# Kernel optimization log

Hardware: AMD Instinct MI355X
Metric: run time of the kernel (lower is better)

## Reference

```python
import jax, jax.numpy as jnp
import numpy as np

NUM_HEADS = 3
WIN = 7            # window_size (square)
PAD = WIN // 2     # conv / v padding


def setup_inputs() -> dict:
    key = jax.random.key(0)
    ks = jax.random.split(key, 8)
    B, C, H, W = 8, 96, 56, 56
    hd = C // NUM_HEADS  # 32
    x = jax.random.normal(ks[0], (B, C, H, W), jnp.float32)
    # qkv 1x1 conv: weight (3C, C), bias (3C,)
    w_qkv = jax.random.normal(ks[1], (3 * C, C), jnp.float32) * (C ** -0.5)
    b_qkv = jax.random.normal(ks[2], (3 * C,), jnp.float32) * 0.01
    fan_in = 2 * hd * WIN * WIN
    w_dm = jax.random.normal(ks[3], (WIN * WIN, 2 * hd, WIN, WIN), jnp.float32) * (fan_in ** -0.5)
    b_dm = jax.random.normal(ks[4], (WIN * WIN,), jnp.float32) * 0.01
    bias_table = jax.random.normal(ks[5], (WIN * WIN, NUM_HEADS), jnp.float32) * 0.02
    # proj 1x1 conv
    w_proj = jax.random.normal(ks[6], (C, C), jnp.float32) * (C ** -0.5)
    b_proj = jax.random.normal(ks[7], (C,), jnp.float32) * 0.01
    return dict(x=x, w_qkv=w_qkv, b_qkv=b_qkv, w_dm=w_dm, b_dm=b_dm,
                bias_table=bias_table, w_proj=w_proj, b_proj=b_proj)


def reference(x, w_qkv, b_qkv, w_dm, b_dm, bias_table, w_proj, b_proj):
    B, C, H, W = x.shape
    nh = NUM_HEADS
    hd = C // nh
    scale = hd ** -0.5

    # qkv 1x1 conv -> (B, 3, nh, hd, H, W)
    qkv = jnp.einsum('oc,bchw->bohw', w_qkv, x) + b_qkv[None, :, None, None]
    qkv = qkv.reshape(B, 3, nh, hd, H, W)
    q, k, v = qkv[:, 0], qkv[:, 1], qkv[:, 2]

    qk = jnp.concatenate([(q * scale).reshape(B * nh, hd, H, W),
                          k.reshape(B * nh, hd, H, W)], axis=1)
    attn = jax.lax.conv_general_dilated(
        qk, w_dm, window_strides=(1, 1), padding=[(PAD, PAD), (PAD, PAD)],
        dimension_numbers=('NCHW', 'OIHW', 'NCHW')) + b_dm[None, :, None, None]
    attn = attn.reshape(B, nh, WIN * WIN, H, W)

    # relative position bias, broadcast over spatial dims
    attn = attn + bias_table.T.reshape(1, nh, WIN * WIN, 1, 1)
    attn = jax.nn.softmax(attn, axis=2)

    # gather sliding windows of v from a zero-padded tensor
    v_pad = jnp.pad(v, ((0, 0), (0, 0), (0, 0), (PAD, PAD), (PAD, PAD)))
    vw = jnp.stack([v_pad[..., i // WIN:i // WIN + H, i % WIN:i % WIN + W]
                    for i in range(WIN * WIN)], axis=3)

    # weighted sum over window dim, merge heads back to channels
    out = jnp.sum(vw * attn[:, :, None], axis=3).reshape(B, C, H, W)

    # output 1x1 projection (dropout p=0 -> identity)
    out = jnp.einsum('oc,bchw->bohw', w_proj, out) + b_proj[None, :, None, None]
    return out
```

## Files before the change

kernel.cpp:

```cpp
#include <hip/hip_runtime.h>
#include <hip/hip_bf16.h>
#include <stdint.h>

#define BATCH 8
#define CCH 96
#define NH 3
#define HD 32
#define HGT 56
#define WID 56
#define HW 3136
#define WIN 7
#define KK 49
#define PADR 3
#define NIMG 24
#define C2 64

typedef const float* fp32p;
typedef __attribute__((ext_vector_type(8))) short bf16x8;
typedef __attribute__((ext_vector_type(16))) float f32x16;
typedef unsigned short ushort_t;

__device__ __forceinline__ float bf2f_bits(unsigned u){ return __uint_as_float(u << 16); }
__device__ __forceinline__ ushort_t f2bf_bits(float f){
  __hip_bfloat16 hb = __float2bfloat16(f);
  return *(ushort_t*)&hb;
}

__global__ void prep_kernel(fp32p w_dm, fp32p b_dm, fp32p bias_table,
                            fp32p w_qkv, fp32p w_proj,
                            __hip_bfloat16* __restrict__ w3, float* __restrict__ bias3,
                            ushort_t* __restrict__ wq3, ushort_t* __restrict__ wp3){
  int t = blockIdx.x * 256 + threadIdx.x;
  if (t < 200704){
    int j   = t & 7;
    int l   = (t >> 3) & 63;
    int mt  = (t >> 9) & 1;
    int cb  = (t >> 10) & 1;
    int pt  = t >> 11;
    int pass = pt / KK, tap = pt % KK;
    int o  = mt*32 + (l & 31);
    int ch = pass*32 + cb*16 + (l >> 5)*8 + j;
    float v = 0.f;
    if (o < KK) v = w_dm[((size_t)(o*C2 + ch))*KK + tap];
    w3[t] = __float2bfloat16(v);
  } else if (t < 200896){
    int t2 = t - 200704;
    int h = t2 >> 6;
    int o = t2 & 63;
    bias3[t2] = (o < KK) ? (b_dm[o] + bias_table[o*NH + h]) : -1e30f;
  } else if (t < 200896 + 27648){
    int i = t - 200896;
    int j = i & 7, l = (i >> 3) & 63;
    int rest = i >> 9;
    int mt = rest % 9, k = rest / 9;
    int o = mt*32 + (l & 31);
    int c = k*16 + (l >> 5)*8 + j;
    wq3[i] = f2bf_bits(w_qkv[o*CCH + c]);
  } else if (t < 200896 + 27648 + 9216){
    int i = t - 200896 - 27648;
    int j = i & 7, l = (i >> 3) & 63;
    int rest = i >> 9;
    int mt = rest % 3, k = rest / 3;
    int o = mt*32 + (l & 31);
    int c = k*16 + (l >> 5)*8 + j;
    wp3[i] = f2bf_bits(w_proj[o*CCH + c]);
  }
}

__global__ __launch_bounds__(256) void xt_kernel(fp32p x, ushort_t* __restrict__ xbf){
  __shared__ float lds[128*97];
  int px0 = blockIdx.x * 128;
  int tid = threadIdx.x;
  #pragma unroll
  for (int it = 0; it < 48; ++it){
    int s = tid + it*256;
    int px = s & 127;
    int c  = s >> 7;
    int gpx = px0 + px;
    int b = gpx / HW, pp = gpx % HW;
    lds[px*97 + c] = x[((size_t)b*CCH + c)*HW + pp];
  }
  __syncthreads();
  #pragma unroll
  for (int it = 0; it < 6; ++it){
    int s = tid + it*256;
    int j  = s % 12;
    int px = s / 12;
    unsigned u[4];
    #pragma unroll
    for (int q = 0; q < 4; ++q){
      float f0 = lds[px*97 + j*8 + 2*q];
      float f1 = lds[px*97 + j*8 + 2*q + 1];
      u[q] = (unsigned)f2bf_bits(f0) | ((unsigned)f2bf_bits(f1) << 16);
    }
    uint4 w4; w4.x=u[0]; w4.y=u[1]; w4.z=u[2]; w4.w=u[3];
    *(uint4*)((char*)xbf + ((size_t)(px0+px)*96 + j*8)*2) = w4;
  }
}

__global__ __launch_bounds__(64) void qkv_kernel(const ushort_t* __restrict__ xbf,
    const ushort_t* __restrict__ wq3, fp32p b_qkv,
    ushort_t* __restrict__ qplane, ushort_t* __restrict__ kplane,
    ushort_t* __restrict__ v2){
  int wid = blockIdx.x;
  int g  = wid / 784;
  int pt = wid % 784;
  int l = threadIdx.x & 63, col = l & 31, hi = l >> 5;
  int px = pt*32 + col;
  int b = px / HW, pp = px % HW;

  bf16x8 B[6];
  const char* bb = (const char*)xbf + (size_t)px*192 + hi*16;
  #pragma unroll
  for (int k = 0; k < 6; ++k) B[k] = *(const bf16x8*)(bb + k*32);

  f32x16 acc[3];
  #pragma unroll
  for (int m = 0; m < 3; ++m)
    #pragma unroll
    for (int r = 0; r < 16; ++r) acc[m][r] = 0.f;

  #pragma unroll
  for (int k = 0; k < 6; ++k){
    #pragma unroll
    for (int m = 0; m < 3; ++m){
      bf16x8 A = *(const bf16x8*)((const char*)wq3 + ((size_t)((k*9 + g*3 + m)*64 + l))*16);
      acc[m] = __builtin_amdgcn_mfma_f32_32x32x16_bf16(A, B[k], acc[m], 0, 0, 0);
    }
  }
  const float scale = 0.17677669529663687f;
  ushort_t* plane = (g == 0) ? qplane : (g == 1 ? kplane : v2);
  #pragma unroll
  for (int m = 0; m < 3; ++m){
    ushort_t* dst = plane + ((size_t)((b*NH + m)*HW + pp))*32;
    #pragma unroll
    for (int q = 0; q < 4; ++q){
      int base = 8*q + 4*hi;
      float v0 = acc[m][q*4+0] + b_qkv[g*96 + m*32 + base + 0];
      float v1 = acc[m][q*4+1] + b_qkv[g*96 + m*32 + base + 1];
      float v2f = acc[m][q*4+2] + b_qkv[g*96 + m*32 + base + 2];
      float v3 = acc[m][q*4+3] + b_qkv[g*96 + m*32 + base + 3];
      if (g == 0){ v0 *= scale; v1 *= scale; v2f *= scale; v3 *= scale; }
      uint2 pk;
      pk.x = (unsigned)f2bf_bits(v0) | ((unsigned)f2bf_bits(v1) << 16);
      pk.y = (unsigned)f2bf_bits(v2f) | ((unsigned)f2bf_bits(v3) << 16);
      *(uint2*)(&dst[base]) = pk;
    }
  }
}

#define MFMA4(Ab, Bb) \
  { _Pragma("unroll") for (int cb = 0; cb < 2; ++cb){ \
      acc[0] = __builtin_amdgcn_mfma_f32_32x32x16_bf16(Ab[cb][0], Bb[cb], acc[0], 0, 0, 0); \
      acc[1] = __builtin_amdgcn_mfma_f32_32x32x16_bf16(Ab[cb][1], Bb[cb], acc[1], 0, 0, 0); \
    } }

#define LOADA(tt, Ab) \
  { const char* An_ = Abase + (size_t)(tt)*4096; \
    _Pragma("unroll") for (int cb = 0; cb < 2; ++cb) \
      _Pragma("unroll") for (int mt = 0; mt < 2; ++mt) \
        Ab[cb][mt] = *(const bf16x8*)(An_ + (cb*2 + mt)*1024); }

#define LOADB(tt, Bb) \
  { int ky_ = (tt) / 7, kx_ = (tt) - ky_*7; \
    int xp_ = nth*32 + col + kx_; if (xp_ > 61) xp_ = 61; \
    int base_ = ((row + ky_)*64 + xp_)*64; \
    int sx_ = (xp_ & 3) ^ ((xp_ >> 2) & 3); \
    _Pragma("unroll") for (int cb = 0; cb < 2; ++cb) \
      Bb[cb] = *(const bf16x8*)(&smem[base_ + ((((cb << 1) | hi) ^ sx_) << 4)]); }

__global__ __launch_bounds__(256, 3) void attn_kernel(
    const ushort_t* __restrict__ qplane, const ushort_t* __restrict__ kplane,
    const __hip_bfloat16* __restrict__ w3, const float* __restrict__ bias3,
    const ushort_t* __restrict__ v2, ushort_t* __restrict__ tmp2){
  __shared__ char smem[49664];

  int bid = blockIdx.x;
  int n  = bid / 28;
  int y0 = (bid % 28) * 2;
  int b = n / NH, head = n % NH;
  int tid = threadIdx.x;
  int l = tid & 63, w = tid >> 6, hi = l >> 5, col = l & 31;
  int row = w >> 1;
  int nth = w & 1;

  f32x16 acc[2];
  #pragma unroll
  for (int r = 0; r < 16; ++r){
    int rowv = (r & 3) + 8*(r >> 2) + 4*hi;
    acc[0][r] = bias3[head*64 + rowv];
    acc[1][r] = bias3[head*64 + 32 + rowv];
  }

  for (int pass = 0; pass < 2; ++pass){
    if (pass) __syncthreads();
    const char* src = (const char*)(pass ? kplane : qplane) + (size_t)n * HW * 64;
    #pragma unroll
    for (int it = 0; it < 8; ++it){
      int s = tid + it*256;
      int c   = s & 3;
      int xp  = (s >> 2) & 63;
      int rw  = s >> 8;
      int gy = y0 - 3 + rw;
      int gx = xp - 3;
      uint4 val = {0,0,0,0};
      if ((unsigned)gy < HGT && (unsigned)gx < WID)
        val = *(const uint4*)(src + (size_t)(gy*WID + gx)*64 + c*16);
      int sw = (c ^ (xp & 3) ^ ((xp >> 2) & 3)) << 4;
      *(uint4*)(&smem[(rw*64 + xp)*64 + sw]) = val;
    }
    __syncthreads();

    const char* Abase = (const char*)w3 + (size_t)pass*KK*4096 + l*16;
    bf16x8 A0[2][2], A1[2][2], B0[2], B1[2];
    LOADA(0, A0); LOADB(0, B0);
    LOADA(1, A1); LOADB(1, B1);
    for (int t = 0; t < 48; t += 2){
      MFMA4(A0, B0);
      LOADA(t+2, A0); LOADB(t+2, B0);
      MFMA4(A1, B1);
      int t3 = (t+3 < KK) ? (t+3) : 48;
      LOADA(t3, A1); LOADB(t3, B1);
    }
    MFMA4(A0, B0);
  }

  ushort_t* Pp = (ushort_t*)&smem[32768];
  {
    float m = -1e30f;
    #pragma unroll
    for (int r = 0; r < 16; ++r){ m = fmaxf(m, acc[0][r]); m = fmaxf(m, acc[1][r]); }
    m = fmaxf(m, __shfl_xor(m, 32));
    float s = 0.f;
    #pragma unroll
    for (int r = 0; r < 16; ++r){
      acc[0][r] = __expf(acc[0][r] - m); s += acc[0][r];
      acc[1][r] = __expf(acc[1][r] - m); s += acc[1][r];
    }
    s += __shfl_xor(s, 32);
    float inv = 1.f / s;
    int pixslot = row*64 + nth*32 + col;
    #pragma unroll
    for (int r = 0; r < 16; ++r){
      int rowv = (r & 3) + 8*(r >> 2) + 4*hi;
      Pp[pixslot*66 + rowv] = f2bf_bits(acc[0][r] * inv);
      int o1 = 32 + rowv;
      if (o1 < KK) Pp[pixslot*66 + o1] = f2bf_bits(acc[1][r] * inv);
    }
  }
  __syncthreads();

  const char* vb = (const char*)v2 + (size_t)n * HW * 64;
  #pragma unroll
  for (int it = 0; it < 8; ++it){
    int s = tid + it*256;
    int xp  = s & 63;
    int c   = (s >> 6) & 3;
    int rw  = s >> 8;
    int gy = y0 - 3 + rw;
    int gx = xp - 3;
    uint4 val = {0,0,0,0};
    if ((unsigned)gy < HGT && (unsigned)gx < WID)
      val = *(const uint4*)(vb + (size_t)(gy*WID + gx)*64 + c*16);
    *(uint4*)(&smem[((c*8 + rw)*64 + xp)*16]) = val;
  }
  __syncthreads();

  int ch2 = tid >> 7;
  int slot = tid & 127;
  int pr = slot >> 6, pxx = slot & 63;
  if (pxx < WID){
    float out[16];
    #pragma unroll
    for (int i = 0; i < 16; ++i) out[i] = 0.f;
    #pragma unroll
    for (int ky = 0; ky < WIN; ++ky){
      #pragma unroll
      for (int kx = 0; kx < WIN; ++kx){
        float pw = bf2f_bits(Pp[slot*66 + ky*7 + kx]);
        int vrow = pr + ky, xp = pxx + kx;
        #pragma unroll
        for (int ci = 0; ci < 2; ++ci){
          int cc = ch2*2 + ci;
          uint4 vv = *(const uint4*)(&smem[((cc*8 + vrow)*64 + xp)*16]);
          unsigned ua[4] = {vv.x, vv.y, vv.z, vv.w};
          #pragma unroll
          for (int q = 0; q < 4; ++q){
            out[ci*8 + 2*q]     = fmaf(pw, __uint_as_float(ua[q] << 16),         out[ci*8 + 2*q]);
            out[ci*8 + 2*q + 1] = fmaf(pw, __uint_as_float(ua[q] & 0xffff0000u), out[ci*8 + 2*q + 1]);
          }
        }
      }
    }
    int pp = (y0 + pr)*WID + pxx;
    ushort_t* dst = tmp2 + ((size_t)(b*HW + pp))*96 + head*32 + ch2*16;
    #pragma unroll
    for (int j2 = 0; j2 < 2; ++j2){
      unsigned u[4];
      #pragma unroll
      for (int q = 0; q < 4; ++q){
        u[q] = (unsigned)f2bf_bits(out[j2*8 + 2*q]) | ((unsigned)f2bf_bits(out[j2*8 + 2*q + 1]) << 16);
      }
      uint4 w4; w4.x=u[0]; w4.y=u[1]; w4.z=u[2]; w4.w=u[3];
      *(uint4*)(&dst[j2*8]) = w4;
    }
  }
}

__global__ __launch_bounds__(64) void proj_kernel(const ushort_t* __restrict__ tmp2,
    const ushort_t* __restrict__ wp3, fp32p b_proj, float* __restrict__ outp){
  int pt = blockIdx.x;
  int l = threadIdx.x & 63, col = l & 31, hi = l >> 5;
  int px = pt*32 + col;
  int b = px / HW, pp = px % HW;

  bf16x8 B[6];
  const char* bb = (const char*)tmp2 + (size_t)px*192 + hi*16;
  #pragma unroll
  for (int k = 0; k < 6; ++k) B[k] = *(const bf16x8*)(bb + k*32);

  f32x16 acc[3];
  #pragma unroll
  for (int m = 0; m < 3; ++m)
    #pragma unroll
    for (int r = 0; r < 16; ++r) acc[m][r] = 0.f;

  #pragma unroll
  for (int k = 0; k < 6; ++k){
    #pragma unroll
    for (int m = 0; m < 3; ++m){
      bf16x8 A = *(const bf16x8*)((const char*)wp3 + ((size_t)((k*3 + m)*64 + l))*16);
      acc[m] = __builtin_amdgcn_mfma_f32_32x32x16_bf16(A, B[k], acc[m], 0, 0, 0);
    }
  }
  #pragma unroll
  for (int m = 0; m < 3; ++m){
    #pragma unroll
    for (int r = 0; r < 16; ++r){
      int o = m*32 + (r & 3) + 8*(r >> 2) + 4*hi;
      outp[((size_t)(b*CCH + o))*HW + pp] = acc[m][r] + b_proj[o];
    }
  }
}

extern "C" void kernel_launch(void* const* d_in, const int* in_sizes, int n_in,
                              void* d_out, int out_size, void* d_ws, size_t ws_size,
                              hipStream_t stream){
  fp32p x          = (fp32p)d_in[0];
  fp32p w_qkv      = (fp32p)d_in[1];
  fp32p b_qkv      = (fp32p)d_in[2];
  fp32p w_dm       = (fp32p)d_in[3];
  fp32p b_dm       = (fp32p)d_in[4];
  fp32p bias_table = (fp32p)d_in[5];
  fp32p w_proj     = (fp32p)d_in[6];
  fp32p b_proj     = (fp32p)d_in[7];

  char* ws = (char*)d_ws;
  const size_t XBF_BYTES   = (size_t)BATCH * HW * 96 * 2;
  const size_t PLANE_BYTES = (size_t)NIMG * HW * 32 * 2;
  const size_t TMP2_BYTES  = (size_t)BATCH * HW * 96 * 2;
  const size_t W3_BYTES    = 200704ull * 2;
  size_t off = 0;
  ushort_t* xbf    = (ushort_t*)(ws + off); off += XBF_BYTES;
  ushort_t* qplane = (ushort_t*)(ws + off); off += PLANE_BYTES;
  ushort_t* kplane = (ushort_t*)(ws + off); off += PLANE_BYTES;
  ushort_t* v2     = (ushort_t*)(ws + off); off += PLANE_BYTES;
  ushort_t* tmp2   = (ushort_t*)(ws + off); off += TMP2_BYTES;
  __hip_bfloat16* w3 = (__hip_bfloat16*)(ws + off); off += W3_BYTES;
  float* bias3     = (float*)(ws + off);    off += 192*4;
  ushort_t* wq3    = (ushort_t*)(ws + off); off += 27648*2;
  ushort_t* wp3    = (ushort_t*)(ws + off); off += 9216*2;

  hipLaunchKernelGGL(prep_kernel, dim3(929), dim3(256), 0, stream,
                     w_dm, b_dm, bias_table, w_qkv, w_proj, w3, bias3, wq3, wp3);
  hipLaunchKernelGGL(xt_kernel, dim3(196), dim3(256), 0, stream, x, xbf);
  hipLaunchKernelGGL(qkv_kernel, dim3(2352), dim3(64), 0, stream,
                     xbf, wq3, b_qkv, qplane, kplane, v2);
  hipLaunchKernelGGL(attn_kernel, dim3(672), dim3(256), 0, stream,
                     qplane, kplane, w3, bias3, v2, tmp2);
  hipLaunchKernelGGL(proj_kernel, dim3(784), dim3(64), 0, stream,
                     tmp2, wp3, b_proj, (float*)d_out);
}
```

Measured before the change: 85.45 us.

## Deepen MFMA operand prefetch and overlap V global loads with softmax

```diff
diff --git a/kernel.cpp b/kernel.cpp
--- a/kernel.cpp
+++ b/kernel.cpp
@@ -173,7 +173,7 @@
     const ushort_t* __restrict__ qplane, const ushort_t* __restrict__ kplane,
     const __hip_bfloat16* __restrict__ w3, const float* __restrict__ bias3,
     const ushort_t* __restrict__ v2, ushort_t* __restrict__ tmp2){
-  __shared__ char smem[49664];
+  __shared__ char smem[50176];
 
   int bid = blockIdx.x;
   int n  = bid / 28;
@@ -212,45 +212,27 @@
     __syncthreads();
 
     const char* Abase = (const char*)w3 + (size_t)pass*KK*4096 + l*16;
-    bf16x8 A0[2][2], A1[2][2], B0[2], B1[2];
+    bf16x8 A0[2][2], A1[2][2], A2[2][2], A3[2][2];
+    bf16x8 B0[2], B1[2], B2[2], B3[2];
     LOADA(0, A0); LOADB(0, B0);
     LOADA(1, A1); LOADB(1, B1);
-    for (int t = 0; t < 48; t += 2){
-      MFMA4(A0, B0);
-      LOADA(t+2, A0); LOADB(t+2, B0);
-      MFMA4(A1, B1);
-      int t3 = (t+3 < KK) ? (t+3) : 48;
-      LOADA(t3, A1); LOADB(t3, B1);
-    }
+    LOADA(2, A2); LOADB(2, B2);
+    LOADA(3, A3); LOADB(3, B3);
+    for (int t = 0; t < 44; t += 4){
+      MFMA4(A0, B0); LOADA(t+4, A0); LOADB(t+4, B0);
+      MFMA4(A1, B1); LOADA(t+5, A1); LOADB(t+5, B1);
+      MFMA4(A2, B2); LOADA(t+6, A2); LOADB(t+6, B2);
+      MFMA4(A3, B3); LOADA(t+7, A3); LOADB(t+7, B3);
+    }
+    MFMA4(A0, B0); LOADA(48, A0); LOADB(48, B0);
+    MFMA4(A1, B1);
+    MFMA4(A2, B2);
+    MFMA4(A3, B3);
     MFMA4(A0, B0);
   }
 
-  ushort_t* Pp = (ushort_t*)&smem[32768];
-  {
-    float m = -1e30f;
-    #pragma unroll
-    for (int r = 0; r < 16; ++r){ m = fmaxf(m, acc[0][r]); m = fmaxf(m, acc[1][r]); }
-    m = fmaxf(m, __shfl_xor(m, 32));
-    float s = 0.f;
-    #pragma unroll
-    for (int r = 0; r < 16; ++r){
-      acc[0][r] = __expf(acc[0][r] - m); s += acc[0][r];
-      acc[1][r] = __expf(acc[1][r] - m); s += acc[1][r];
-    }
-    s += __shfl_xor(s, 32);
-    float inv = 1.f / s;
-    int pixslot = row*64 + nth*32 + col;
-    #pragma unroll
-    for (int r = 0; r < 16; ++r){
-      int rowv = (r & 3) + 8*(r >> 2) + 4*hi;
-      Pp[pixslot*66 + rowv] = f2bf_bits(acc[0][r] * inv);
-      int o1 = 32 + rowv;
-      if (o1 < KK) Pp[pixslot*66 + o1] = f2bf_bits(acc[1][r] * inv);
-    }
-  }
-  __syncthreads();
-
   const char* vb = (const char*)v2 + (size_t)n * HW * 64;
+  uint4 vreg[8];
   #pragma unroll
   for (int it = 0; it < 8; ++it){
     int s = tid + it*256;
@@ -262,7 +244,47 @@
     uint4 val = {0,0,0,0};
     if ((unsigned)gy < HGT && (unsigned)gx < WID)
       val = *(const uint4*)(vb + (size_t)(gy*WID + gx)*64 + c*16);
-    *(uint4*)(&smem[((c*8 + rw)*64 + xp)*16]) = val;
+    vreg[it] = val;
+  }
+
+  ushort_t* Pp = (ushort_t*)&smem[32768];
+  {
+    float m = -1e30f;
+    #pragma unroll
+    for (int r = 0; r < 16; ++r){ m = fmaxf(m, acc[0][r]); m = fmaxf(m, acc[1][r]); }
+    m = fmaxf(m, __shfl_xor(m, 32));
+    float s = 0.f;
+    #pragma unroll
+    for (int r = 0; r < 16; ++r){
+      acc[0][r] = __expf(acc[0][r] - m); s += acc[0][r];
+      acc[1][r] = __expf(acc[1][r] - m); s += acc[1][r];
+    }
+    s += __shfl_xor(s, 32);
+    float inv = 1.f / s;
+    int pixslot = row*64 + nth*32 + col;
+    ushort_t* Pr = Pp + pixslot*68;
+    #pragma unroll
+    for (int q = 0; q < 4; ++q){
+      int base = 8*q + 4*hi;
+      uint2 pk0;
+      pk0.x = (unsigned)f2bf_bits(acc[0][q*4+0]*inv) | ((unsigned)f2bf_bits(acc[0][q*4+1]*inv) << 16);
+      pk0.y = (unsigned)f2bf_bits(acc[0][q*4+2]*inv) | ((unsigned)f2bf_bits(acc[0][q*4+3]*inv) << 16);
+      *(uint2*)(&Pr[base]) = pk0;
+      uint2 pk1;
+      pk1.x = (unsigned)f2bf_bits(acc[1][q*4+0]*inv) | ((unsigned)f2bf_bits(acc[1][q*4+1]*inv) << 16);
+      pk1.y = (unsigned)f2bf_bits(acc[1][q*4+2]*inv) | ((unsigned)f2bf_bits(acc[1][q*4+3]*inv) << 16);
+      *(uint2*)(&Pr[32 + base]) = pk1;
+    }
+  }
+  __syncthreads();
+
+  #pragma unroll
+  for (int it = 0; it < 8; ++it){
+    int s = tid + it*256;
+    int xp  = s & 63;
+    int c   = (s >> 6) & 3;
+    int rw  = s >> 8;
+    *(uint4*)(&smem[((c*8 + rw)*64 + xp)*16]) = vreg[it];
   }
   __syncthreads();
 
@@ -277,7 +299,7 @@
     for (int ky = 0; ky < WIN; ++ky){
       #pragma unroll
       for (int kx = 0; kx < WIN; ++kx){
-        float pw = bf2f_bits(Pp[slot*66 + ky*7 + kx]);
+        float pw = bf2f_bits(Pp[slot*68 + ky*7 + kx]);
         int vrow = pr + ky, xp = pxx + kx;
         #pragma unroll
         for (int ci = 0; ci < 2; ++ci){
```

After: 151.6 us. 77.4% more time.
